# Performance work log

Measured on AMD Instinct MI355X. Metric: run time of the kernel, lower is better.

The kernel has to match this reference:

```python
import jax, jax.numpy as jnp
import numpy as np

B, C, H, W = 4, 16, 256, 256
O = 32
KH = KW = 3
PAD = 1


def setup_inputs() -> dict:
    key = jax.random.key(0)
    ks = jax.random.split(key, 6)
    d_in = C * KH * KW          # 144
    d_out = O * KH * KW         # 288
    s1 = 1.0 / np.sqrt(d_in)
    s2 = 1.0 / np.sqrt(O)
    return {
        "x": jax.random.normal(ks[0], (B, C, H, W), dtype=jnp.float32),
        "W1": jax.random.uniform(ks[1], (O, d_in), jnp.float32, -s1, s1),
        "b1": jax.random.uniform(ks[2], (O,), jnp.float32, -s1, s1),
        "W2": jax.random.uniform(ks[3], (d_out, O), jnp.float32, -s2, s2),
        "b2": jax.random.uniform(ks[4], (d_out,), jnp.float32, -s2, s2),
        "bias": jax.random.uniform(ks[5], (O,), jnp.float32, -s1, s1),
    }


def _unfold(x):
    """im2col matching torch F.unfold ordering (c, kh, kw): -> [B, H*W, C*KH*KW]."""
    b, c, h, w = x.shape
    xp = jnp.pad(x, ((0, 0), (0, 0), (PAD, PAD), (PAD, PAD)))
    # stack the KH*KW shifted views: [B, C, KH*KW, H, W]
    shifts = [xp[:, :, i:i + h, j:j + w] for i in range(KH) for j in range(KW)]
    p = jnp.stack(shifts, axis=2)
    # -> [B, H, W, C, KH*KW] -> [B, L, C*KH*KW]  (c-major, then (i,j))
    p = p.transpose(0, 3, 4, 1, 2)
    return p.reshape(b, h * w, c * KH * KW)


def reference(x, W1, b1, W2, b2, bias):
    b, c, h, w = x.shape
    L = h * w
    feat = _unfold(x)                                   # [B, L, C*9]
    # per-pixel kernel generator MLP
    hid = jnp.tanh(jnp.einsum('blf,of->blo', feat, W1) + b1)          # [B, L, O]
    kern = jnp.einsum('blo,go->blg', hid, W2) + b2                    # [B, L, O*9]
    kern = kern.reshape(b, L, O, KH * KW)                             # [B, L, O, 9]
    # contract per-pixel kernel with its patch (channels summed):
    # out[b,l,o] = sum_{c,i,j} K[b,l,o,ij] * P[b,l,c,ij]
    patch_c = feat.reshape(b, L, c, KH * KW).sum(axis=2)              # [B, L, 9]
    out = jnp.einsum('blok,blk->blo', kern, patch_c)                  # [B, L, O]
    out = out.transpose(0, 2, 1).reshape(b, O, h, w)
    return out + bias[None, :, None, None]
```

## Files before the change

kernel.cpp:

```cpp
#include <hip/hip_runtime.h>

#define CC 16
#define OO 32
#define LL 65536

typedef __attribute__((ext_vector_type(8))) short bf16x8;
typedef __attribute__((ext_vector_type(4))) float f32x4;
typedef __attribute__((ext_vector_type(4))) int   i32x4;

static __device__ __forceinline__ ushort f2b(float f) {
    union { float f; unsigned u; } v; v.f = f;
    return (ushort)((v.u + 0x7fff + ((v.u >> 16) & 1)) >> 16);
}
static __device__ __forceinline__ unsigned pk2(float fl, float fh) {
    unsigned ul = __float_as_uint(fl) + 0x8000u;
    unsigned uh = __float_as_uint(fh) + 0x8000u;
    return __builtin_amdgcn_perm(uh, ul, 0x07060302);
}
static __device__ __forceinline__ unsigned pkt(float fl, float fh) {
    return __builtin_amdgcn_perm(__float_as_uint(fh), __float_as_uint(fl), 0x07060302);
}

__global__ void prepass(const float* __restrict__ W1, const float* __restrict__ b1,
                        const float* __restrict__ W2, const float* __restrict__ b2,
                        const float* __restrict__ bias,
                        ushort* __restrict__ w1f, ushort* __restrict__ w2f) {
    int idx = blockIdx.x * 256 + threadIdx.x;
    if (idx < 5120) {
        int f = idx >> 9, lane = (idx >> 3) & 63, j = idx & 7;
        int ks = f >> 1, ot = f & 1, lm = lane & 15, g = lane >> 4;
        int o = ot * 16 + lm, kk = ks * 32 + g * 8 + j;
        int r = kk >> 4, c = kk & 15;
        float v = (kk < 144) ? W1[o * 144 + c * 9 + r] : (kk == 144 ? b1[o] : 0.f);
        w1f[idx] = f2b(v);
    } else if (idx < 15360) {
        int i2 = idx - 5120;
        int f = i2 >> 9, lane = (i2 >> 3) & 63, j = i2 & 7;
        int ks = f >> 1, ot = f & 1, lm = lane & 15, g = lane >> 4;
        int o = ot * 16 + lm, kk = ks * 32 + g * 8 + j;
        float v;
        if      (kk < 288) v = W2[o * 288 + kk];
        else if (kk < 297) v = b2[o * 9 + (kk - 288)];
        else if (kk == 297) v = bias[o];
        else               v = 0.f;
        w2f[i2] = f2b(v);
    }
}

__global__ __launch_bounds__(256, 2) void dynaconv_mfma(
    const float* __restrict__ x, const ushort* __restrict__ w1f,
    const ushort* __restrict__ w2f, float* __restrict__ out)
{
    __shared__ __align__(16) ushort xs[4][260][24];
    __shared__ __align__(16) float  S[4][260];
    __shared__ __align__(16) float  hidT[4][16][36];

    const int tid  = threadIdx.x;
    const int wv   = tid >> 6;
    const int lane = tid & 63;
    const int g    = lane >> 4;
    const int lm   = lane & 15;

    const int vbid = (blockIdx.x & 7) * 64 + (blockIdx.x >> 3);
    const int b    = vbid >> 7;
    const int h0   = (vbid & 127) * 2;

    bf16x8 W1R[10], W2R[20];
#pragma unroll
    for (int f = 0; f < 10; ++f) W1R[f] = *(const bf16x8*)(w1f + (f * 64 + lane) * 8);
#pragma unroll
    for (int f = 0; f < 20; ++f) W2R[f] = *(const bf16x8*)(w2f + (f * 64 + lane) * 8);

    const float* xb = x + b * (CC * LL);
    {
        int offr[4]; bool okr[4];
#pragma unroll
        for (int r = 0; r < 4; ++r) {
            const int hh = h0 - 1 + r;
            okr[r] = (unsigned)hh < 256u;
            offr[r] = (okr[r] ? hh : 0) * 256 + tid;
        }
        float sr[4] = {0.f, 0.f, 0.f, 0.f};
#pragma unroll
        for (int cp = 0; cp < 8; ++cp) {
            const float* p0 = xb + (2 * cp) * LL;
            const float* p1 = p0 + LL;
#pragma unroll
            for (int r = 0; r < 4; ++r) {
                float va = p0[offr[r]], vb = p1[offr[r]];
                va = okr[r] ? va : 0.f; vb = okr[r] ? vb : 0.f;
                sr[r] += va + vb;
                *(unsigned*)&xs[r][tid + 1][2 * cp] = pk2(va, vb);
            }
        }
#pragma unroll
        for (int r = 0; r < 4; ++r) S[r][tid + 1] = sr[r];
        if (tid < 128) { int r = tid >> 5, side = (tid >> 4) & 1, c = tid & 15; xs[r][side * 257][c] = 0; }
        if (tid < 8)   S[tid >> 1][(tid & 1) * 257] = 0.f;
    }
    __syncthreads();

    int soff[5];
#pragma unroll
    for (int ks = 0; ks < 5; ++ks) {
        int r = 2 * ks + (g >> 1); if (r > 8) r = 8;
        int r3 = (r * 11) >> 5, rm = r - 3 * r3;
        soff[ks] = (r3 * 260 + rm + lm) * 24 + (g & 1) * 8;
    }
    const ushort* xsf = &xs[0][0][0];

    for (int hr = 0; hr < 2; ++hr) {
        const int hb = hr * (260 * 24);
#pragma unroll
        for (int t = 0; t < 4; ++t) {
            const int w0t = wv * 64 + t * 16;
            const int tb = w0t * 24 + hb;

            f32x4 a1[2] = {{0.f,0.f,0.f,0.f},{0.f,0.f,0.f,0.f}};
#pragma unroll
            for (int ks = 0; ks < 5; ++ks) {
                bf16x8 ff = *(const bf16x8*)(xsf + soff[ks] + tb);
                if (ks == 4) {
                    i32x4 wd = *(i32x4*)&ff;
                    wd[0] = (g < 2) ? wd[0] : (g == 2 ? 0x3F80 : 0);
                    wd[1] = (g < 2) ? wd[1] : 0;
                    wd[2] = (g < 2) ? wd[2] : 0;
                    wd[3] = (g < 2) ? wd[3] : 0;
                    ff = *(bf16x8*)&wd;
                }
                a1[0] = __builtin_amdgcn_mfma_f32_16x16x32_bf16(W1R[2 * ks],     ff, a1[0], 0, 0, 0);
                a1[1] = __builtin_amdgcn_mfma_f32_16x16x32_bf16(W1R[2 * ks + 1], ff, a1[1], 0, 0, 0);
            }

#pragma unroll
            for (int ot = 0; ot < 2; ++ot)
#pragma unroll
                for (int q = 0; q < 4; ++q) {
                    float e = __expf(2.f * a1[ot][q]);
                    hidT[wv][lm][ot * 16 + g * 4 + q] = 1.f - 2.f / (e + 1.f);
                }
            f32x4 h0v = *(const f32x4*)&hidT[wv][lm][g * 8];
            f32x4 h1v = *(const f32x4*)&hidT[wv][lm][g * 8 + 4];

            float pcv[9];
#pragma unroll
            for (int r = 0; r < 9; ++r) pcv[r] = S[r / 3 + hr][w0t + lm + (r % 3)];

            f32x4 a2[2] = {{0.f,0.f,0.f,0.f},{0.f,0.f,0.f,0.f}};
#pragma unroll
            for (int ks = 0; ks < 9; ++ks) {
                const float p = pcv[ks];
                i32x4 wd;
                wd[0] = (int)pkt(h0v[0] * p, h0v[1] * p);
                wd[1] = (int)pkt(h0v[2] * p, h0v[3] * p);
                wd[2] = (int)pkt(h1v[0] * p, h1v[1] * p);
                wd[3] = (int)pkt(h1v[2] * p, h1v[3] * p);
                bf16x8 ff2 = *(bf16x8*)&wd;
                a2[0] = __builtin_amdgcn_mfma_f32_16x16x32_bf16(W2R[2 * ks],     ff2, a2[0], 0, 0, 0);
                a2[1] = __builtin_amdgcn_mfma_f32_16x16x32_bf16(W2R[2 * ks + 1], ff2, a2[1], 0, 0, 0);
            }
            {
                i32x4 wd;
                wd[0] = (g == 0) ? (int)pk2(pcv[0], pcv[1]) : ((g == 1) ? (int)pk2(pcv[8], 1.f) : 0);
                wd[1] = (g == 0) ? (int)pk2(pcv[2], pcv[3]) : 0;
                wd[2] = (g == 0) ? (int)pk2(pcv[4], pcv[5]) : 0;
                wd[3] = (g == 0) ? (int)pk2(pcv[6], pcv[7]) : 0;
                bf16x8 ff2 = *(bf16x8*)&wd;
                a2[0] = __builtin_amdgcn_mfma_f32_16x16x32_bf16(W2R[18], ff2, a2[0], 0, 0, 0);
                a2[1] = __builtin_amdgcn_mfma_f32_16x16x32_bf16(W2R[19], ff2, a2[1], 0, 0, 0);
            }

            float* ob = out + b * (OO * LL) + (h0 + hr) * 256 + w0t + lm;
#pragma unroll
            for (int ot = 0; ot < 2; ++ot)
#pragma unroll
                for (int q = 0; q < 4; ++q)
                    ob[(ot * 16 + g * 4 + q) * LL] = a2[ot][q];
        }
    }
}

extern "C" void kernel_launch(void* const* d_in, const int* in_sizes, int n_in,
                              void* d_out, int out_size, void* d_ws, size_t ws_size,
                              hipStream_t stream) {
    const float* x    = (const float*)d_in[0];
    const float* W1   = (const float*)d_in[1];
    const float* b1   = (const float*)d_in[2];
    const float* W2   = (const float*)d_in[3];
    const float* b2   = (const float*)d_in[4];
    const float* bias = (const float*)d_in[5];
    float* out = (float*)d_out;

    ushort* w1f = (ushort*)d_ws;
    ushort* w2f = w1f + 5120;

    prepass<<<60, 256, 0, stream>>>(W1, b1, W2, b2, bias, w1f, w2f);
    dynaconv_mfma<<<512, 256, 0, stream>>>(x, w1f, w2f, out);
}
```

Before: 28.01 us.

## Process one row per block, stream W2 fragments from global, raise occupancy

Each block now handles a single output row instead of two, so the grid doubles to 1024 blocks and the shared halo buffers shrink to three rows with a tighter 16-element padding. W2 fragments are no longer held in 20 register vectors; they are loaded from global memory (expected to hit cache) inside the MFMA loop, and launch bounds ask for 4 blocks per CU. The aim is more occupancy and latency hiding. In exchange, the halo rows of x are reloaded more often (3 input rows per output row instead of 4 per 2), W2 loads are repeated, and the 16-ushort LDS row stride may cause bank conflicts.

```diff
diff --git a/kernel.cpp b/kernel.cpp
--- a/kernel.cpp
+++ b/kernel.cpp
@@ -47,12 +47,12 @@
     }
 }
 
-__global__ __launch_bounds__(256, 2) void dynaconv_mfma(
+__global__ __launch_bounds__(256, 4) void dynaconv_mfma(
     const float* __restrict__ x, const ushort* __restrict__ w1f,
     const ushort* __restrict__ w2f, float* __restrict__ out)
 {
-    __shared__ __align__(16) ushort xs[4][260][24];
-    __shared__ __align__(16) float  S[4][260];
+    __shared__ __align__(16) ushort xs[3][258][16];
+    __shared__ __align__(16) float  S[3][258];
     __shared__ __align__(16) float  hidT[4][16][36];
 
     const int tid  = threadIdx.x;
@@ -61,32 +61,30 @@
     const int g    = lane >> 4;
     const int lm   = lane & 15;
 
-    const int vbid = (blockIdx.x & 7) * 64 + (blockIdx.x >> 3);
-    const int b    = vbid >> 7;
-    const int h0   = (vbid & 127) * 2;
-
-    bf16x8 W1R[10], W2R[20];
+    const int vbid = (blockIdx.x & 7) * 128 + (blockIdx.x >> 3);
+    const int b    = vbid >> 8;
+    const int h    = vbid & 255;
+
+    bf16x8 W1R[10];
 #pragma unroll
     for (int f = 0; f < 10; ++f) W1R[f] = *(const bf16x8*)(w1f + (f * 64 + lane) * 8);
-#pragma unroll
-    for (int f = 0; f < 20; ++f) W2R[f] = *(const bf16x8*)(w2f + (f * 64 + lane) * 8);
 
     const float* xb = x + b * (CC * LL);
     {
-        int offr[4]; bool okr[4];
-#pragma unroll
-        for (int r = 0; r < 4; ++r) {
-            const int hh = h0 - 1 + r;
+        int offr[3]; bool okr[3];
+#pragma unroll
+        for (int r = 0; r < 3; ++r) {
+            const int hh = h - 1 + r;
             okr[r] = (unsigned)hh < 256u;
             offr[r] = (okr[r] ? hh : 0) * 256 + tid;
         }
-        float sr[4] = {0.f, 0.f, 0.f, 0.f};
+        float sr[3] = {0.f, 0.f, 0.f};
 #pragma unroll
         for (int cp = 0; cp < 8; ++cp) {
             const float* p0 = xb + (2 * cp) * LL;
             const float* p1 = p0 + LL;
 #pragma unroll
-            for (int r = 0; r < 4; ++r) {
+            for (int r = 0; r < 3; ++r) {
                 float va = p0[offr[r]], vb = p1[offr[r]];
                 va = okr[r] ? va : 0.f; vb = okr[r] ? vb : 0.f;
                 sr[r] += va + vb;
@@ -94,9 +92,10 @@
             }
         }
 #pragma unroll
-        for (int r = 0; r < 4; ++r) S[r][tid + 1] = sr[r];
-        if (tid < 128) { int r = tid >> 5, side = (tid >> 4) & 1, c = tid & 15; xs[r][side * 257][c] = 0; }
-        if (tid < 8)   S[tid >> 1][(tid & 1) * 257] = 0.f;
+        for (int r = 0; r < 3; ++r) S[r][tid + 1] = sr[r];
+        if (tid < 48) { int r = tid >> 4, side = (tid >> 3) & 1, cw = tid & 7;
+                        *(unsigned*)&xs[r][side * 257][2 * cw] = 0u; }
+        if (tid < 6)  S[tid >> 1][(tid & 1) * 257] = 0.f;
     }
     __syncthreads();
 
@@ -105,78 +104,80 @@
     for (int ks = 0; ks < 5; ++ks) {
         int r = 2 * ks + (g >> 1); if (r > 8) r = 8;
         int r3 = (r * 11) >> 5, rm = r - 3 * r3;
-        soff[ks] = (r3 * 260 + rm + lm) * 24 + (g & 1) * 8;
+        soff[ks] = (r3 * 258 + rm + lm) * 16 + (g & 1) * 8;
     }
     const ushort* xsf = &xs[0][0][0];
-
-    for (int hr = 0; hr < 2; ++hr) {
-        const int hb = hr * (260 * 24);
-#pragma unroll
-        for (int t = 0; t < 4; ++t) {
-            const int w0t = wv * 64 + t * 16;
-            const int tb = w0t * 24 + hb;
-
-            f32x4 a1[2] = {{0.f,0.f,0.f,0.f},{0.f,0.f,0.f,0.f}};
-#pragma unroll
-            for (int ks = 0; ks < 5; ++ks) {
-                bf16x8 ff = *(const bf16x8*)(xsf + soff[ks] + tb);
-                if (ks == 4) {
-                    i32x4 wd = *(i32x4*)&ff;
-                    wd[0] = (g < 2) ? wd[0] : (g == 2 ? 0x3F80 : 0);
-                    wd[1] = (g < 2) ? wd[1] : 0;
-                    wd[2] = (g < 2) ? wd[2] : 0;
-                    wd[3] = (g < 2) ? wd[3] : 0;
-                    ff = *(bf16x8*)&wd;
-                }
-                a1[0] = __builtin_amdgcn_mfma_f32_16x16x32_bf16(W1R[2 * ks],     ff, a1[0], 0, 0, 0);
-                a1[1] = __builtin_amdgcn_mfma_f32_16x16x32_bf16(W1R[2 * ks + 1], ff, a1[1], 0, 0, 0);
+    const ushort* w2g = w2f + lane * 8;
+
+#pragma unroll
+    for (int t = 0; t < 4; ++t) {
+        const int w0t = wv * 64 + t * 16;
+        const int tb = w0t * 16;
+
+        f32x4 a1[2] = {{0.f,0.f,0.f,0.f},{0.f,0.f,0.f,0.f}};
+#pragma unroll
+        for (int ks = 0; ks < 5; ++ks) {
+            bf16x8 ff = *(const bf16x8*)(xsf + soff[ks] + tb);
+            if (ks == 4) {
+                i32x4 wd = *(i32x4*)&ff;
+                wd[0] = (g < 2) ? wd[0] : (g == 2 ? 0x3F80 : 0);
+                wd[1] = (g < 2) ? wd[1] : 0;
+                wd[2] = (g < 2) ? wd[2] : 0;
+                wd[3] = (g < 2) ? wd[3] : 0;
+                ff = *(bf16x8*)&wd;
             }
-
-#pragma unroll
-            for (int ot = 0; ot < 2; ++ot)
-#pragma unroll
-                for (int q = 0; q < 4; ++q) {
-                    float e = __expf(2.f * a1[ot][q]);
-                    hidT[wv][lm][ot * 16 + g * 4 + q] = 1.f - 2.f / (e + 1.f);
-                }
-            f32x4 h0v = *(const f32x4*)&hidT[wv][lm][g * 8];
-            f32x4 h1v = *(const f32x4*)&hidT[wv][lm][g * 8 + 4];
-
-            float pcv[9];
-#pragma unroll
-            for (int r = 0; r < 9; ++r) pcv[r] = S[r / 3 + hr][w0t + lm + (r % 3)];
-
-            f32x4 a2[2] = {{0.f,0.f,0.f,0.f},{0.f,0.f,0.f,0.f}};
-#pragma unroll
-            for (int ks = 0; ks < 9; ++ks) {
-                const float p = pcv[ks];
-                i32x4 wd;
-                wd[0] = (int)pkt(h0v[0] * p, h0v[1] * p);
-                wd[1] = (int)pkt(h0v[2] * p, h0v[3] * p);
-                wd[2] = (int)pkt(h1v[0] * p, h1v[1] * p);
-                wd[3] = (int)pkt(h1v[2] * p, h1v[3] * p);
-                bf16x8 ff2 = *(bf16x8*)&wd;
-                a2[0] = __builtin_amdgcn_mfma_f32_16x16x32_bf16(W2R[2 * ks],     ff2, a2[0], 0, 0, 0);
-                a2[1] = __builtin_amdgcn_mfma_f32_16x16x32_bf16(W2R[2 * ks + 1], ff2, a2[1], 0, 0, 0);
+            a1[0] = __builtin_amdgcn_mfma_f32_16x16x32_bf16(W1R[2 * ks],     ff, a1[0], 0, 0, 0);
+            a1[1] = __builtin_amdgcn_mfma_f32_16x16x32_bf16(W1R[2 * ks + 1], ff, a1[1], 0, 0, 0);
+        }
+
+#pragma unroll
+        for (int ot = 0; ot < 2; ++ot)
+#pragma unroll
+            for (int q = 0; q < 4; ++q) {
+                float e = __expf(2.f * a1[ot][q]);
+                hidT[wv][lm][ot * 16 + g * 4 + q] = 1.f - 2.f / (e + 1.f);
             }
-            {
-                i32x4 wd;
-                wd[0] = (g == 0) ? (int)pk2(pcv[0], pcv[1]) : ((g == 1) ? (int)pk2(pcv[8], 1.f) : 0);
-                wd[1] = (g == 0) ? (int)pk2(pcv[2], pcv[3]) : 0;
-                wd[2] = (g == 0) ? (int)pk2(pcv[4], pcv[5]) : 0;
-                wd[3] = (g == 0) ? (int)pk2(pcv[6], pcv[7]) : 0;
-                bf16x8 ff2 = *(bf16x8*)&wd;
-                a2[0] = __builtin_amdgcn_mfma_f32_16x16x32_bf16(W2R[18], ff2, a2[0], 0, 0, 0);
-                a2[1] = __builtin_amdgcn_mfma_f32_16x16x32_bf16(W2R[19], ff2, a2[1], 0, 0, 0);
-            }
-
-            float* ob = out + b * (OO * LL) + (h0 + hr) * 256 + w0t + lm;
-#pragma unroll
-            for (int ot = 0; ot < 2; ++ot)
-#pragma unroll
-                for (int q = 0; q < 4; ++q)
-                    ob[(ot * 16 + g * 4 + q) * LL] = a2[ot][q];
-        }
+        f32x4 h0v = *(const f32x4*)&hidT[wv][lm][g * 8];
+        f32x4 h1v = *(const f32x4*)&hidT[wv][lm][g * 8 + 4];
+
+        float pcv[9];
+#pragma unroll
+        for (int r = 0; r < 9; ++r) pcv[r] = S[r / 3][w0t + lm + (r % 3)];
+
+        f32x4 a2[2] = {{0.f,0.f,0.f,0.f},{0.f,0.f,0.f,0.f}};
+#pragma unroll
+        for (int ks = 0; ks < 9; ++ks) {
+            bf16x8 bm0 = *(const bf16x8*)(w2g + (2 * ks) * 512);
+            bf16x8 bm1 = *(const bf16x8*)(w2g + (2 * ks + 1) * 512);
+            const float p = pcv[ks];
+            i32x4 wd;
+            wd[0] = (int)pkt(h0v[0] * p, h0v[1] * p);
+            wd[1] = (int)pkt(h0v[2] * p, h0v[3] * p);
+            wd[2] = (int)pkt(h1v[0] * p, h1v[1] * p);
+            wd[3] = (int)pkt(h1v[2] * p, h1v[3] * p);
+            bf16x8 ff2 = *(bf16x8*)&wd;
+            a2[0] = __builtin_amdgcn_mfma_f32_16x16x32_bf16(bm0, ff2, a2[0], 0, 0, 0);
+            a2[1] = __builtin_amdgcn_mfma_f32_16x16x32_bf16(bm1, ff2, a2[1], 0, 0, 0);
+        }
+        {
+            bf16x8 bm0 = *(const bf16x8*)(w2g + 18 * 512);
+            bf16x8 bm1 = *(const bf16x8*)(w2g + 19 * 512);
+            i32x4 wd;
+            wd[0] = (g == 0) ? (int)pk2(pcv[0], pcv[1]) : ((g == 1) ? (int)pk2(pcv[8], 1.f) : 0);
+            wd[1] = (g == 0) ? (int)pk2(pcv[2], pcv[3]) : 0;
+            wd[2] = (g == 0) ? (int)pk2(pcv[4], pcv[5]) : 0;
+            wd[3] = (g == 0) ? (int)pk2(pcv[6], pcv[7]) : 0;
+            bf16x8 ff2 = *(bf16x8*)&wd;
+            a2[0] = __builtin_amdgcn_mfma_f32_16x16x32_bf16(bm0, ff2, a2[0], 0, 0, 0);
+            a2[1] = __builtin_amdgcn_mfma_f32_16x16x32_bf16(bm1, ff2, a2[1], 0, 0, 0);
+        }
+
+        float* ob = out + b * (OO * LL) + h * 256 + w0t + lm;
+#pragma unroll
+        for (int ot = 0; ot < 2; ++ot)
+#pragma unroll
+            for (int q = 0; q < 4; ++q)
+                ob[(ot * 16 + g * 4 + q) * LL] = a2[ot][q];
     }
 }
 
@@ -195,5 +196,5 @@
     ushort* w2f = w1f + 5120;
 
     prepass<<<60, 256, 0, stream>>>(W1, b1, W2, b2, bias, w1f, w2f);
-    dynaconv_mfma<<<512, 256, 0, stream>>>(x, w1f, w2f, out);
-}
+    dynaconv_mfma<<<1024, 256, 0, stream>>>(x, w1f, w2f, out);
+}
```

Result: slower. 35.33 us (+26.1%).
